# Performance work log

Hardware: AMD Instinct MI355X
Metric: run time of the kernel (lower is better)

The kernel has to match this reference:

```python
import jax, jax.numpy as jnp
import numpy as np

B, S, D_IN, D_OUT, H = 4, 2048, 1024, 1024, 16
HD = D_OUT // H  # head_dim = 64


def setup_inputs() -> dict:
    key = jax.random.key(0)
    ks = jax.random.split(key, 6)
    scale_in = 1.0 / np.sqrt(D_IN)
    scale_out = 1.0 / np.sqrt(D_OUT)
    return {
        "x": jax.random.normal(ks[0], (B, S, D_IN), dtype=jnp.float32),
        "Wq": jax.random.uniform(ks[1], (D_IN, D_OUT), jnp.float32, -scale_in, scale_in),
        "Wk": jax.random.uniform(ks[2], (D_IN, D_OUT), jnp.float32, -scale_in, scale_in),
        "Wv": jax.random.uniform(ks[3], (D_IN, D_OUT), jnp.float32, -scale_in, scale_in),
        "Wo": jax.random.uniform(ks[4], (D_OUT, D_OUT), jnp.float32, -scale_out, scale_out),
        "bo": jax.random.uniform(ks[5], (D_OUT,), jnp.float32, -scale_out, scale_out),
    }


def reference(x, Wq, Wk, Wv, Wo, bo):
    b, s, _ = x.shape
    # QKV projections (no bias), split into heads: [b, h, s, hd]
    q = (x @ Wq).reshape(b, s, H, HD).transpose(0, 2, 1, 3)
    k = (x @ Wk).reshape(b, s, H, HD).transpose(0, 2, 1, 3)
    v = (x @ Wv).reshape(b, s, H, HD).transpose(0, 2, 1, 3)
    # scores [b, h, s, s], causal mask (upper triangle -> -inf), scaled softmax
    scores = jnp.einsum("bhqd,bhkd->bhqk", q, k)
    causal = jnp.triu(jnp.ones((s, s), dtype=bool), k=1)
    scores = jnp.where(causal, -jnp.inf, scores)
    attn = jax.nn.softmax(scores / np.sqrt(HD), axis=-1)
    # dropout p=0.0 (eval-equivalent): identity
    ctx = jnp.einsum("bhqk,bhkd->bqhd", attn, v).reshape(b, s, D_OUT)
    return ctx @ Wo + bo
```

## Files before the change

### kernel.cpp

```cpp
#include <hip/hip_runtime.h>
#include <hip/hip_bf16.h>

typedef __hip_bfloat16 bf16;
typedef __attribute__((ext_vector_type(4))) float f32x4;
typedef __attribute__((ext_vector_type(8))) short s16x8;
typedef __attribute__((ext_vector_type(4))) short s16x4;
typedef __attribute__((ext_vector_type(4))) unsigned int u32x4;

#define B_    4
#define S_    2048
#define H_    16
#define HD_   64
#define DIN   1024
#define DOUT  1024

__device__ __forceinline__ void gld16(const void* g, void* l) {
  __builtin_amdgcn_global_load_lds((const __attribute__((address_space(1))) void*)g,
                                   (__attribute__((address_space(3))) void*)l, 16, 0, 0);
}

__device__ __forceinline__ short bfbits(float f) {
  bf16 h = __float2bfloat16(f);
  short r; __builtin_memcpy(&r, &h, 2); return r;
}

__device__ __forceinline__ unsigned pk2(float lo, float hi) {
  return (unsigned)(unsigned short)bfbits(lo) | ((unsigned)(unsigned short)bfbits(hi) << 16);
}

__global__ __launch_bounds__(256) void cvt_f32_bf16(const float* __restrict__ in,
                                                    bf16* __restrict__ out, int n4) {
  int i = blockIdx.x * 256 + threadIdx.x;
  if (i >= n4) return;
  float4 v = reinterpret_cast<const float4*>(in)[i];
  s16x4 o = { bfbits(v.x), bfbits(v.y), bfbits(v.z), bfbits(v.w) };
  reinterpret_cast<s16x4*>(out)[i] = o;
}

__global__ __launch_bounds__(256) void transpose_w_bf16(
    const float* __restrict__ W0, const float* __restrict__ W1,
    const float* __restrict__ W2, const float* __restrict__ W3,
    bf16* __restrict__ T0, bf16* __restrict__ T1,
    bf16* __restrict__ T2, bf16* __restrict__ T3) {
  const float* W; bf16* T;
  switch (blockIdx.z) {
    case 0:  W = W0; T = T0; break;
    case 1:  W = W1; T = T1; break;
    case 2:  W = W2; T = T2; break;
    default: W = W3; T = T3; break;
  }
  __shared__ float tile[32][33];
  const int n0 = blockIdx.x * 32, k0 = blockIdx.y * 32;
  const int tx = threadIdx.x & 31, ty = threadIdx.x >> 5;
#pragma unroll
  for (int i = 0; i < 4; ++i)
    tile[ty + i * 8][tx] = W[(size_t)(k0 + ty + i * 8) * DOUT + n0 + tx];
  __syncthreads();
#pragma unroll
  for (int i = 0; i < 4; ++i)
    T[(size_t)(n0 + ty + i * 8) * DIN + k0 + tx] = __float2bfloat16(tile[tx][ty + i * 8]);
}

template <int KDIM>
__device__ __forceinline__ void gemm128_mainloop(
    const bf16* __restrict__ A, const bf16* __restrict__ Bt,
    int brow, int bcol, bf16* Al, bf16* Bl, f32x4 acc[4][4]) {
  const int tid = threadIdx.x;
  const int lane = tid & 63;
  const int wr = (tid >> 6) >> 1, wc = (tid >> 6) & 1;
  const int lq = lane & 15, lg = lane >> 4;
  const int r0 = tid >> 2, kg = tid & 3;

  for (int k0 = 0; k0 < KDIM; k0 += 32) {
    gld16(A  + (size_t)(brow + r0)      * KDIM + k0 + kg * 8, (char*)Al + tid * 16);
    gld16(A  + (size_t)(brow + r0 + 64) * KDIM + k0 + kg * 8, (char*)Al + (tid + 256) * 16);
    gld16(Bt + (size_t)(bcol + r0)      * KDIM + k0 + kg * 8, (char*)Bl + tid * 16);
    gld16(Bt + (size_t)(bcol + r0 + 64) * KDIM + k0 + kg * 8, (char*)Bl + (tid + 256) * 16);
    __syncthreads();
    s16x8 af[4], bff[4];
#pragma unroll
    for (int m = 0; m < 4; ++m)
      af[m] = *(const s16x8*)((const char*)Al + (wr * 64 + m * 16 + lq) * 64 + lg * 16);
#pragma unroll
    for (int n = 0; n < 4; ++n)
      bff[n] = *(const s16x8*)((const char*)Bl + (wc * 64 + n * 16 + lq) * 64 + lg * 16);
#pragma unroll
    for (int m = 0; m < 4; ++m)
#pragma unroll
      for (int n = 0; n < 4; ++n)
        acc[m][n] = __builtin_amdgcn_mfma_f32_16x16x32_bf16(af[m], bff[n], acc[m][n], 0, 0, 0);
    __syncthreads();
  }
}

__global__ __launch_bounds__(256) void gemm_qkv(
    const bf16* __restrict__ A,
    const bf16* __restrict__ Wqt, const bf16* __restrict__ Wkt, const bf16* __restrict__ Wvt,
    bf16* __restrict__ Qo, bf16* __restrict__ Ko, bf16* __restrict__ Vo) {
  __shared__ alignas(16) bf16 Al[128 * 32];
  __shared__ alignas(16) bf16 Bl[128 * 32];
  const int z = blockIdx.z;
  const bf16* Bt = (z == 0) ? Wqt : (z == 1) ? Wkt : Wvt;
  bf16* Out = (z == 0) ? Qo : (z == 1) ? Ko : Vo;
  const float scale = (z == 0) ? 0.125f : 1.0f;
  const int brow = blockIdx.x * 128, bcol = blockIdx.y * 128;
  f32x4 acc[4][4];
  const f32x4 z4 = {0.f, 0.f, 0.f, 0.f};
#pragma unroll
  for (int m = 0; m < 4; ++m)
#pragma unroll
    for (int n = 0; n < 4; ++n) acc[m][n] = z4;
  gemm128_mainloop<1024>(A, Bt, brow, bcol, Al, Bl, acc);
  const int lane = threadIdx.x & 63;
  const int wr = (threadIdx.x >> 6) >> 1, wc = (threadIdx.x >> 6) & 1;
  const int lq = lane & 15, lg = lane >> 4;
#pragma unroll
  for (int m = 0; m < 4; ++m) {
#pragma unroll
    for (int n = 0; n < 4; ++n) {
      const int col = bcol + wc * 64 + n * 16 + lq;
      const int h = col >> 6, hd = col & 63;
#pragma unroll
      for (int r = 0; r < 4; ++r) {
        const int row = brow + wr * 64 + m * 16 + lg * 4 + r;
        const int b = row >> 11, s = row & 2047;
        Out[(((size_t)(b * H_ + h) * S_ + s) << 6) + hd] = __float2bfloat16(acc[m][n][r] * scale);
      }
    }
  }
}

__global__ __launch_bounds__(256, 4) void attn_fwd(
    const bf16* __restrict__ Qg, const bf16* __restrict__ Kg, const bf16* __restrict__ Vg,
    bf16* __restrict__ ctx) {
  __shared__ alignas(16) bf16 Ks[128 * 64];
  __shared__ alignas(16) bf16 Vt[64 * 128];
  const int orig = blockIdx.y * 32 + blockIdx.x;
  const int sw = ((orig & 7) << 8) | (orig >> 3);
  const int qi = sw & 31, bh = sw >> 5;
  const int tid = threadIdx.x, wave = tid >> 6, lane = tid & 63;
  const int lq = lane & 15, lg = lane >> 4;
  const size_t base = (size_t)bh * S_ * HD_;
  const int qt0 = qi * 64;
  const int qw0 = qt0 + wave * 16;

  s16x8 qf[2];
  {
    const bf16* qp = Qg + base + (size_t)(qw0 + lq) * HD_ + lg * 8;
    qf[0] = *(const s16x8*)qp;
    qf[1] = *(const s16x8*)(qp + 32);
  }
  const f32x4 z4 = {0.f, 0.f, 0.f, 0.f};
  f32x4 o[4];
#pragma unroll
  for (int nf = 0; nf < 4; ++nf) o[nf] = z4;
  float mrow = -1e30f, lrow = 0.f;

  const int n_kv = (qt0 + 63) / 128 + 1;
  for (int kt = 0; kt < n_kv; ++kt) {
    const int k0 = kt * 128;
#pragma unroll
    for (int i = 0; i < 4; ++i) {
      const int c = tid + i * 256;
      const int key = c >> 3;
      const int s8 = (c & 7) ^ (key & 7);
      gld16(Kg + base + (size_t)(k0 + key) * HD_ + s8 * 8, (char*)Ks + c * 16);
    }
    const int key0 = (tid & 31) * 4, hdg = tid >> 5;
    s16x8 v0, v1, v2, v3;
    {
      const bf16* vp = Vg + base + (size_t)(k0 + key0) * HD_ + hdg * 8;
      v0 = *(const s16x8*)vp;
      v1 = *(const s16x8*)(vp + HD_);
      v2 = *(const s16x8*)(vp + 2 * HD_);
      v3 = *(const s16x8*)(vp + 3 * HD_);
    }
    __syncthreads();
#pragma unroll
    for (int j = 0; j < 8; ++j) {
      const int hd = hdg * 8 + j;
      const int byte = ((hd * 128 + key0) * 2) ^ ((hd & 15) << 4);
      s16x4 wv = { v0[j], v1[j], v2[j], v3[j] };
      *(s16x4*)((char*)Vt + byte) = wv;
    }

    f32x4 sc[8];
#pragma unroll
    for (int n = 0; n < 8; ++n) sc[n] = z4;
    __builtin_amdgcn_s_setprio(1);
#pragma unroll
    for (int ks = 0; ks < 2; ++ks) {
#pragma unroll
      for (int n = 0; n < 8; ++n) {
        const int key = n * 16 + lq;
        const int byte = (key * 128 + ks * 64 + lg * 16) ^ ((key & 7) << 4);
        const s16x8 kf = *(const s16x8*)((const char*)Ks + byte);
        sc[n] = __builtin_amdgcn_mfma_f32_16x16x32_bf16(kf, qf[ks], sc[n], 0, 0, 0);
      }
    }
    __builtin_amdgcn_s_setprio(0);
    if (k0 + 127 > qw0) {
      const int gq = qw0 + lq;
#pragma unroll
      for (int n = 0; n < 8; ++n) {
        const int kb = k0 + n * 16 + lg * 4;
#pragma unroll
        for (int r = 0; r < 4; ++r)
          if (kb + r > gq) sc[n][r] = -1e30f;
      }
    }
    float mn[8];
#pragma unroll
    for (int n = 0; n < 8; ++n)
      mn[n] = fmaxf(fmaxf(sc[n][0], sc[n][1]), fmaxf(sc[n][2], sc[n][3]));
    float pm = fmaxf(fmaxf(fmaxf(mn[0], mn[1]), fmaxf(mn[2], mn[3])),
                     fmaxf(fmaxf(mn[4], mn[5]), fmaxf(mn[6], mn[7])));
    pm = fmaxf(pm, __shfl_xor(pm, 16, 64));
    pm = fmaxf(pm, __shfl_xor(pm, 32, 64));
    const float mnew = fmaxf(mrow, pm);
    const float alpha = __expf(mrow - mnew);
    mrow = mnew;
    float sn[8];
#pragma unroll
    for (int n = 0; n < 8; ++n) {
#pragma unroll
      for (int r = 0; r < 4; ++r) sc[n][r] = __expf(sc[n][r] - mnew);
      sn[n] = (sc[n][0] + sc[n][1]) + (sc[n][2] + sc[n][3]);
    }
    float rs = ((sn[0] + sn[1]) + (sn[2] + sn[3])) + ((sn[4] + sn[5]) + (sn[6] + sn[7]));
    rs += __shfl_xor(rs, 16, 64);
    rs += __shfl_xor(rs, 32, 64);
    lrow = lrow * alpha + rs;
    s16x8 pb[4];
#pragma unroll
    for (int w = 0; w < 4; ++w) {
      const unsigned Aw = pk2(sc[2 * w][0], sc[2 * w][1]);
      const unsigned Bw = pk2(sc[2 * w][2], sc[2 * w][3]);
      const unsigned Cw = pk2(sc[2 * w + 1][0], sc[2 * w + 1][1]);
      const unsigned Dw = pk2(sc[2 * w + 1][2], sc[2 * w + 1][3]);
      const int src0 = lq + ((lg & 1) << 5);
      const int src1 = src0 + 16;
      const unsigned sA0 = __shfl(Aw, src0, 64), sC0 = __shfl(Cw, src0, 64);
      const unsigned sB0 = __shfl(Bw, src0, 64), sD0 = __shfl(Dw, src0, 64);
      const unsigned sA1 = __shfl(Aw, src1, 64), sC1 = __shfl(Cw, src1, 64);
      const unsigned sB1 = __shfl(Bw, src1, 64), sD1 = __shfl(Dw, src1, 64);
      const bool loh = (lg < 2);
      const u32x4 pw = { loh ? sA0 : sC0, loh ? sB0 : sD0,
                         loh ? sA1 : sC1, loh ? sB1 : sD1 };
      pb[w] = __builtin_bit_cast(s16x8, pw);
    }
#pragma unroll
    for (int nf = 0; nf < 4; ++nf)
#pragma unroll
      for (int r = 0; r < 4; ++r) o[nf][r] *= alpha;
    __syncthreads();
    __builtin_amdgcn_s_setprio(1);
#pragma unroll
    for (int w = 0; w < 4; ++w) {
      const s16x8 pbw = pb[w];
#pragma unroll
      for (int nf = 0; nf < 4; ++nf) {
        const int hd = nf * 16 + lq;
        const int bbyte = ((hd * 128 + w * 32 + lg * 8) * 2) ^ ((hd & 15) << 4);
        const s16x8 vf = *(const s16x8*)((const char*)Vt + bbyte);
        o[nf] = __builtin_amdgcn_mfma_f32_16x16x32_bf16(vf, pbw, o[nf], 0, 0, 0);
      }
    }
    __builtin_amdgcn_s_setprio(0);
  }
  const int b = bh >> 4, h = bh & 15;
  const float rinv = __builtin_amdgcn_rcpf(lrow);
  bf16* cp = ctx + (size_t)(b * S_ + qw0 + lq) * DOUT + h * HD_ + lg * 4;
#pragma unroll
  for (int nf = 0; nf < 4; ++nf) {
    s16x4 ov = { bfbits(o[nf][0] * rinv), bfbits(o[nf][1] * rinv),
                 bfbits(o[nf][2] * rinv), bfbits(o[nf][3] * rinv) };
    *(s16x4*)(cp + nf * 16) = ov;
  }
}

__global__ __launch_bounds__(256) void gemm_outproj(
    const bf16* __restrict__ A, const bf16* __restrict__ Wot,
    const float* __restrict__ bo, float* __restrict__ out) {
  __shared__ alignas(16) bf16 Al[128 * 32];
  __shared__ alignas(16) bf16 Bl[128 * 32];
  const int brow = blockIdx.x * 128, bcol = blockIdx.y * 128;
  f32x4 acc[4][4];
  const f32x4 z4 = {0.f, 0.f, 0.f, 0.f};
#pragma unroll
  for (int m = 0; m < 4; ++m)
#pragma unroll
    for (int n = 0; n < 4; ++n) acc[m][n] = z4;
  gemm128_mainloop<1024>(A, Wot, brow, bcol, Al, Bl, acc);
  const int lane = threadIdx.x & 63;
  const int wr = (threadIdx.x >> 6) >> 1, wc = (threadIdx.x >> 6) & 1;
  const int lq = lane & 15, lg = lane >> 4;
#pragma unroll
  for (int m = 0; m < 4; ++m) {
#pragma unroll
    for (int n = 0; n < 4; ++n) {
      const int col = bcol + wc * 64 + n * 16 + lq;
      const float bias = bo[col];
#pragma unroll
      for (int r = 0; r < 4; ++r) {
        const int row = brow + wr * 64 + m * 16 + lg * 4 + r;
        out[(size_t)row * DOUT + col] = acc[m][n][r] + bias;
      }
    }
  }
}

extern "C" void kernel_launch(void* const* d_in, const int* in_sizes, int n_in,
                              void* d_out, int out_size, void* d_ws, size_t ws_size,
                              hipStream_t stream) {
  (void)in_sizes; (void)n_in; (void)out_size; (void)ws_size;
  const float* x  = (const float*)d_in[0];
  const float* Wq = (const float*)d_in[1];
  const float* Wk = (const float*)d_in[2];
  const float* Wv = (const float*)d_in[3];
  const float* Wo = (const float*)d_in[4];
  const float* bo = (const float*)d_in[5];
  float* out = (float*)d_out;

  char* ws = (char*)d_ws;
  bf16* xb  = (bf16*)(ws);
  bf16* Wqt = (bf16*)(ws + (16u << 20));
  bf16* Wkt = (bf16*)(ws + (18u << 20));
  bf16* Wvt = (bf16*)(ws + (20u << 20));
  bf16* Wot = (bf16*)(ws + (22u << 20));
  bf16* Qb  = (bf16*)(ws + (24u << 20));
  bf16* Kb  = (bf16*)(ws + (40u << 20));
  bf16* Vb  = (bf16*)(ws + (56u << 20));
  bf16* ctx = (bf16*)(ws + (72u << 20));

  cvt_f32_bf16<<<dim3(8192), dim3(256), 0, stream>>>(x, xb, (B_ * S_ * DIN) / 4);
  transpose_w_bf16<<<dim3(32, 32, 4), dim3(256), 0, stream>>>(Wq, Wk, Wv, Wo,
                                                              Wqt, Wkt, Wvt, Wot);
  gemm_qkv<<<dim3(64, 8, 3), dim3(256), 0, stream>>>(xb, Wqt, Wkt, Wvt, Qb, Kb, Vb);
  attn_fwd<<<dim3(32, 64), dim3(256), 0, stream>>>(Qb, Kb, Vb, ctx);
  gemm_outproj<<<dim3(64, 8), dim3(256), 0, stream>>>(ctx, Wot, bo, out);
}
```

Before: 308.0 us.

## Pair causal query tiles per block, prefetch next K/V, defer softmax rescale

Each attention block now handles two query tiles, pr and 31-pr, so every block does the same 17 KV iterations and causal load imbalance disappears, with half as many blocks launched. The K/V loads for the next iteration are issued after the barrier so they overlap the PV MFMAs. Online-softmax rescaling is skipped when the new row max exceeds the running max by at most 8, which saves the exp and the accumulator multiplies but lets exp values grow up to e^8 before normalisation. The risk is lower occupancy from fewer blocks, and possible bf16 precision loss in P.

Measured after the change: 335.9 us. 1.09x slower.

```diff
diff --git a/kernel.cpp b/kernel.cpp
--- a/kernel.cpp
+++ b/kernel.cpp
@@ -135,30 +135,22 @@
     bf16* __restrict__ ctx) {
   __shared__ alignas(16) bf16 Ks[128 * 64];
   __shared__ alignas(16) bf16 Vt[64 * 128];
-  const int orig = blockIdx.y * 32 + blockIdx.x;
-  const int sw = ((orig & 7) << 8) | (orig >> 3);
-  const int qi = sw & 31, bh = sw >> 5;
+  const int orig = blockIdx.x;
+  const int sw = ((orig & 7) << 7) | (orig >> 3);
+  const int bh = sw >> 4, pr = sw & 15;
+  const int t0 = pr, t1 = 31 - pr;
+  const int nk0 = (pr >> 1) + 1;
   const int tid = threadIdx.x, wave = tid >> 6, lane = tid & 63;
   const int lq = lane & 15, lg = lane >> 4;
   const size_t base = (size_t)bh * S_ * HD_;
-  const int qt0 = qi * 64;
-  const int qw0 = qt0 + wave * 16;
-
+  const int b = bh >> 4, h = bh & 15;
+
+  const int key0 = (tid & 31) * 4, hdg = tid >> 5;
+  s16x8 v0, v1, v2, v3;
   s16x8 qf[2];
-  {
-    const bf16* qp = Qg + base + (size_t)(qw0 + lq) * HD_ + lg * 8;
-    qf[0] = *(const s16x8*)qp;
-    qf[1] = *(const s16x8*)(qp + 32);
-  }
-  const f32x4 z4 = {0.f, 0.f, 0.f, 0.f};
-  f32x4 o[4];
-#pragma unroll
-  for (int nf = 0; nf < 4; ++nf) o[nf] = z4;
-  float mrow = -1e30f, lrow = 0.f;
-
-  const int n_kv = (qt0 + 63) / 128 + 1;
-  for (int kt = 0; kt < n_kv; ++kt) {
-    const int k0 = kt * 128;
+
+  auto item_k0 = [&](int it) { return ((it < nk0) ? it : it - nk0) * 128; };
+  auto stage_K = [&](int k0) {
 #pragma unroll
     for (int i = 0; i < 4; ++i) {
       const int c = tid + i * 256;
@@ -166,15 +158,35 @@
       const int s8 = (c & 7) ^ (key & 7);
       gld16(Kg + base + (size_t)(k0 + key) * HD_ + s8 * 8, (char*)Ks + c * 16);
     }
-    const int key0 = (tid & 31) * 4, hdg = tid >> 5;
-    s16x8 v0, v1, v2, v3;
-    {
-      const bf16* vp = Vg + base + (size_t)(k0 + key0) * HD_ + hdg * 8;
-      v0 = *(const s16x8*)vp;
-      v1 = *(const s16x8*)(vp + HD_);
-      v2 = *(const s16x8*)(vp + 2 * HD_);
-      v3 = *(const s16x8*)(vp + 3 * HD_);
-    }
+  };
+  auto load_V = [&](int k0) {
+    const bf16* vp = Vg + base + (size_t)(k0 + key0) * HD_ + hdg * 8;
+    v0 = *(const s16x8*)vp;
+    v1 = *(const s16x8*)(vp + HD_);
+    v2 = *(const s16x8*)(vp + 2 * HD_);
+    v3 = *(const s16x8*)(vp + 3 * HD_);
+  };
+  auto load_qf = [&](int tile) {
+    const bf16* qp = Qg + base + (size_t)(tile * 64 + wave * 16 + lq) * HD_ + lg * 8;
+    qf[0] = *(const s16x8*)qp;
+    qf[1] = *(const s16x8*)(qp + 32);
+  };
+
+  const f32x4 z4 = {0.f, 0.f, 0.f, 0.f};
+  f32x4 o[4];
+#pragma unroll
+  for (int nf = 0; nf < 4; ++nf) o[nf] = z4;
+  float mrow = -1e30f, lrow = 0.f;
+
+  load_qf(t0);
+  stage_K(0);
+  load_V(0);
+
+  for (int it = 0; it < 17; ++it) {
+    const int ctile = (it < nk0) ? t0 : t1;
+    const int k0 = item_k0(it);
+    const int qw0 = ctile * 64 + wave * 16;
+
     __syncthreads();
 #pragma unroll
     for (int j = 0; j < 8; ++j) {
@@ -217,14 +229,18 @@
                      fmaxf(fmaxf(mn[4], mn[5]), fmaxf(mn[6], mn[7])));
     pm = fmaxf(pm, __shfl_xor(pm, 16, 64));
     pm = fmaxf(pm, __shfl_xor(pm, 32, 64));
-    const float mnew = fmaxf(mrow, pm);
-    const float alpha = __expf(mrow - mnew);
-    mrow = mnew;
+    const bool defer = __all(pm - mrow <= 8.0f);
+    float alpha = 1.0f;
+    if (!defer) {
+      const float mnew = fmaxf(mrow, pm);
+      alpha = __expf(mrow - mnew);
+      mrow = mnew;
+    }
     float sn[8];
 #pragma unroll
     for (int n = 0; n < 8; ++n) {
 #pragma unroll
-      for (int r = 0; r < 4; ++r) sc[n][r] = __expf(sc[n][r] - mnew);
+      for (int r = 0; r < 4; ++r) sc[n][r] = __expf(sc[n][r] - mrow);
       sn[n] = (sc[n][0] + sc[n][1]) + (sc[n][2] + sc[n][3]);
     }
     float rs = ((sn[0] + sn[1]) + (sn[2] + sn[3])) + ((sn[4] + sn[5]) + (sn[6] + sn[7]));
@@ -249,11 +265,18 @@
                          loh ? sA1 : sC1, loh ? sB1 : sD1 };
       pb[w] = __builtin_bit_cast(s16x8, pw);
     }
-#pragma unroll
-    for (int nf = 0; nf < 4; ++nf)
-#pragma unroll
-      for (int r = 0; r < 4; ++r) o[nf][r] *= alpha;
+    if (!defer) {
+#pragma unroll
+      for (int nf = 0; nf < 4; ++nf)
+#pragma unroll
+        for (int r = 0; r < 4; ++r) o[nf][r] *= alpha;
+    }
     __syncthreads();
+    if (it + 1 < 17) {
+      const int nk0_ = item_k0(it + 1);
+      stage_K(nk0_);
+      load_V(nk0_);
+    }
     __builtin_amdgcn_s_setprio(1);
 #pragma unroll
     for (int w = 0; w < 4; ++w) {
@@ -267,15 +290,22 @@
       }
     }
     __builtin_amdgcn_s_setprio(0);
-  }
-  const int b = bh >> 4, h = bh & 15;
-  const float rinv = __builtin_amdgcn_rcpf(lrow);
-  bf16* cp = ctx + (size_t)(b * S_ + qw0 + lq) * DOUT + h * HD_ + lg * 4;
-#pragma unroll
-  for (int nf = 0; nf < 4; ++nf) {
-    s16x4 ov = { bfbits(o[nf][0] * rinv), bfbits(o[nf][1] * rinv),
-                 bfbits(o[nf][2] * rinv), bfbits(o[nf][3] * rinv) };
-    *(s16x4*)(cp + nf * 16) = ov;
+    if (it + 1 == nk0 || it + 1 == 17) {
+      const float rinv = __builtin_amdgcn_rcpf(lrow);
+      bf16* cp = ctx + (size_t)(b * S_ + qw0 + lq) * DOUT + h * HD_ + lg * 4;
+#pragma unroll
+      for (int nf = 0; nf < 4; ++nf) {
+        s16x4 ov = { bfbits(o[nf][0] * rinv), bfbits(o[nf][1] * rinv),
+                     bfbits(o[nf][2] * rinv), bfbits(o[nf][3] * rinv) };
+        *(s16x4*)(cp + nf * 16) = ov;
+      }
+      if (it + 1 == nk0) {
+#pragma unroll
+        for (int nf = 0; nf < 4; ++nf) o[nf] = z4;
+        mrow = -1e30f; lrow = 0.f;
+        load_qf(t1);
+      }
+    }
   }
 }
 
@@ -337,6 +367,6 @@
   transpose_w_bf16<<<dim3(32, 32, 4), dim3(256), 0, stream>>>(Wq, Wk, Wv, Wo,
                                                               Wqt, Wkt, Wvt, Wot);
   gemm_qkv<<<dim3(64, 8, 3), dim3(256), 0, stream>>>(xb, Wqt, Wkt, Wvt, Qb, Kb, Vb);
-  attn_fwd<<<dim3(32, 64), dim3(256), 0, stream>>>(Qb, Kb, Vb, ctx);
+  attn_fwd<<<dim3(1024), dim3(256), 0, stream>>>(Qb, Kb, Vb, ctx);
   gemm_outproj<<<dim3(64, 8), dim3(256), 0, stream>>>(ctx, Wot, bo, out);
 }
```
